# Optimization experiments

Measured on AMD Instinct MI355X. Metric: run time of the kernel, lower is better.

The kernel has to match this reference:

```python
import jax, jax.numpy as jnp
import numpy as np

B, S, D, H = 4, 2048, 2048, 16
HD = D // H  # 128, even -> odd-padding branch in rotate_pos_encode is inactive


def rope(x, base):
    # x: [..., S, Dh], Dh even. freqs_len = (Dh+1)//2 == Dh//2
    Dh = x.shape[-1]
    half = (Dh + 1) // 2
    f = 1.0 / base ** (jnp.arange(half, dtype=jnp.float32) / half)
    ang = jnp.arange(x.shape[-2], dtype=jnp.float32)[:, None] * f[None, :]  # [S, half]
    cos, sin = jnp.cos(ang), jnp.sin(ang)
    xr = x.reshape(*x.shape[:-1], half, 2)
    x0, x1 = xr[..., 0], xr[..., 1]
    # complex multiply (x0 + i x1) * (cos + i sin)
    out = jnp.stack([x0 * cos - x1 * sin, x0 * sin + x1 * cos], axis=-1)
    return out.reshape(x.shape)


def setup_inputs() -> dict:
    key = jax.random.key(0)
    ks = jax.random.split(key, 8)
    sc = 1.0 / np.sqrt(D)
    return {
        "subject_tokens": jax.random.normal(ks[0], (B, S, D), jnp.float32),
        "object_tokens": jax.random.normal(ks[1], (B, S, D), jnp.float32),
        "wq": jax.random.normal(ks[2], (D, D), jnp.float32) * sc,
        "bq": jnp.zeros((D,), jnp.float32),
        "wk": jax.random.normal(ks[3], (D, D), jnp.float32) * sc,
        "bk": jnp.zeros((D,), jnp.float32),
        "wv": jax.random.normal(ks[4], (D, D), jnp.float32) * sc,
        "bv": jnp.zeros((D,), jnp.float32),
        "wc": jax.random.normal(ks[5], (D, D), jnp.float32) * sc,
        "bc": jnp.zeros((D,), jnp.float32),
        "rotate_base": 10000.0,
        "msk": jnp.tril(jnp.ones((S, S), jnp.int32)),  # causal mask
    }


def _split_heads(x):
    # [B, S, D] -> [B, H, S, HD]
    return x.reshape(*x.shape[:-1], H, HD).swapaxes(-3, -2)


def reference(subject_tokens, object_tokens, wq, bq, wk, bk, wv, bv, wc, bc, rotate_base, msk):
    q = _split_heads(subject_tokens @ wq + bq)
    k = _split_heads(object_tokens @ wk + bk)
    v = _split_heads(object_tokens @ wv + bv)
    q = rope(q, rotate_base)
    k = rope(k, rotate_base)
    a = jnp.einsum('bhsd,bhtd->bhst', q, k) / jnp.sqrt(jnp.float32(HD))
    a = jnp.where(msk == 0, jnp.float32(-1e9), a)
    a = jax.nn.softmax(a, axis=-1)  # dropout is identity in eval mode
    c = jnp.einsum('bhst,bhtd->bhsd', a, v)
    c = c.swapaxes(-3, -2).reshape(*subject_tokens.shape[:-1], H * HD)
    return c @ wc + bc
```

## Files before the change

kernel.cpp:

```cpp
#include <hip/hip_runtime.h>
#include <hip/hip_bf16.h>
#include <math.h>

#define BB 4
#define SS 2048
#define DD 2048
#define HH 16
#define HDIM 128
#define MM (BB * SS)

typedef __attribute__((ext_vector_type(8))) __bf16 bf16x8;
typedef __attribute__((ext_vector_type(4))) float f32x4;

__device__ __forceinline__ void gload_lds16(const void* g, void* l) {
  __builtin_amdgcn_global_load_lds(
      (const __attribute__((address_space(1))) void*)g,
      (__attribute__((address_space(3))) void*)l, 16, 0, 0);
}

__device__ __forceinline__ unsigned short f2us(float x) {
  __hip_bfloat16 h = __float2bfloat16(x);
  return *reinterpret_cast<unsigned short*>(&h);
}

__global__ void detect_cfg(const unsigned int* __restrict__ subj,
                           const unsigned short* __restrict__ rb,
                           unsigned int* __restrict__ cfg) {
  if (threadIdx.x != 0) return;
  int hits = 0;
  for (int i = 0; i < 128; ++i) {
    unsigned int e = (subj[i] >> 7) & 0xFF;
    if (e >= 0x68 && e <= 0x88) ++hits;
  }
  int flagF32 = (hits < 64) ? 1 : 0;

  float c32 = __uint_as_float(((const unsigned int*)rb)[0]);
  float c64;
  {
    unsigned long long u = ((const unsigned long long*)rb)[0];
    c64 = (float)__longlong_as_double((long long)u);
  }
  float c16 = __uint_as_float(((unsigned int)rb[0]) << 16);
  auto ok = [](float x) { return x >= 2.0f && x <= 1.0e8f; };
  float base;
  if (flagF32)
    base = ok(c32) ? c32 : (ok(c64) ? c64 : (ok(c16) ? c16 : 10000.0f));
  else
    base = ok(c16) ? c16 : (ok(c32) ? c32 : (ok(c64) ? c64 : 10000.0f));

  cfg[0] = (unsigned int)flagF32;
  ((float*)cfg)[1] = base;
}

__global__ __launch_bounds__(256) void conv_bf16(
    const void* __restrict__ src, unsigned short* __restrict__ dst,
    long long n8, const unsigned int* __restrict__ cfg) {
  long long i = (long long)blockIdx.x * 256 + threadIdx.x;
  if (i >= n8) return;
  if (cfg[0]) {
    const float4* s = (const float4*)src;
    float4 a = s[2 * i], b = s[2 * i + 1];
    uint4 o;
    o.x = ((unsigned)f2us(a.y) << 16) | f2us(a.x);
    o.y = ((unsigned)f2us(a.w) << 16) | f2us(a.z);
    o.z = ((unsigned)f2us(b.y) << 16) | f2us(b.x);
    o.w = ((unsigned)f2us(b.w) << 16) | f2us(b.z);
    ((uint4*)dst)[i] = o;
  } else {
    ((uint4*)dst)[i] = ((const uint4*)src)[i];
  }
}

__global__ __launch_bounds__(256) void rope_table(
    const unsigned int* __restrict__ cfg, float* __restrict__ cosT,
    float* __restrict__ sinT) {
  int id = blockIdx.x * 256 + threadIdx.x;
  float base = ((const float*)cfg)[1];
  if (!(base >= 2.0f && base <= 1.0e8f)) base = 10000.0f;
  int s = id >> 6, p = id & 63;
  float f = 1.0f / powf(base, (float)p * (1.0f / 64.0f));
  if (!isfinite(f)) f = 0.0f;
  float ang = (float)s * f;
  cosT[id] = cosf(ang);
  sinT[id] = sinf(ang);
}

__global__ __launch_bounds__(256) void prep_weightT(
    const void* __restrict__ in, unsigned short* __restrict__ out,
    const unsigned int* __restrict__ cfg) {
  __shared__ unsigned short tile[64][65];
  const int tid = threadIdx.x;
  const int bx = blockIdx.x * 64;
  const int by = blockIdx.y * 64;
  const int isF32 = cfg[0];
#pragma unroll
  for (int i = 0; i < 4; ++i) {
    int r = (tid >> 4) + i * 16;
    int c4 = (tid & 15) * 4;
    if (isF32) {
      float4 v = *(const float4*)((const float*)in + (size_t)(by + r) * DD +
                                  bx + c4);
      tile[c4 + 0][r] = f2us(v.x);
      tile[c4 + 1][r] = f2us(v.y);
      tile[c4 + 2][r] = f2us(v.z);
      tile[c4 + 3][r] = f2us(v.w);
    } else {
      ushort4 v = *(const ushort4*)((const unsigned short*)in +
                                    (size_t)(by + r) * DD + bx + c4);
      tile[c4 + 0][r] = v.x;
      tile[c4 + 1][r] = v.y;
      tile[c4 + 2][r] = v.z;
      tile[c4 + 3][r] = v.w;
    }
  }
  __syncthreads();
#pragma unroll
  for (int i = 0; i < 4; ++i) {
    int c = (tid >> 4) + i * 16;
    int r4 = (tid & 15) * 4;
    ushort4 v;
    v.x = tile[c][r4 + 0];
    v.y = tile[c][r4 + 1];
    v.z = tile[c][r4 + 2];
    v.w = tile[c][r4 + 3];
    *(ushort4*)(out + (size_t)(bx + c) * DD + by + r4) = v;
  }
}

__global__ __launch_bounds__(256) void gemm_nt(
    const __hip_bfloat16* __restrict__ A, const __hip_bfloat16* __restrict__ Bt,
    const __hip_bfloat16* __restrict__ bias, const float* __restrict__ ropeCos,
    const float* __restrict__ ropeSin, void* __restrict__ outv, int mode,
    const unsigned int* __restrict__ cfg) {
  __shared__ __hip_bfloat16 Asm_[128 * 64];
  __shared__ __hip_bfloat16 Bsm_[128 * 64];
  const int tid = threadIdx.x;
  const int wave = tid >> 6, lane = tid & 63;
  const int fl = lane & 15, quad = lane >> 4;
  const int wr = (wave >> 1) * 64, wc = (wave & 1) * 64;
  const int m0 = blockIdx.y * 128, n0 = blockIdx.x * 128;

  const __hip_bfloat16* Ab = A + (size_t)m0 * DD;
  const __hip_bfloat16* Bb = Bt + (size_t)n0 * DD;

  f32x4 acc[4][4] = {};

  for (int k0 = 0; k0 < DD; k0 += 64) {
    __syncthreads();
#pragma unroll
    for (int j = 0; j < 4; ++j) {
      int slot = j * 256 + tid;
      int row = slot >> 3;
      int c8 = ((slot & 7) ^ (row & 7)) << 3;
      int dst = j * 4096 + wave * 1024;
      gload_lds16(Ab + (size_t)row * DD + (k0 + c8), (char*)Asm_ + dst);
      gload_lds16(Bb + (size_t)row * DD + (k0 + c8), (char*)Bsm_ + dst);
    }
    asm volatile("s_waitcnt vmcnt(0)" ::: "memory");
    __syncthreads();

#pragma unroll
    for (int kk = 0; kk < 2; ++kk) {
      bf16x8 af[4], bfv[4];
#pragma unroll
      for (int mb = 0; mb < 4; ++mb) {
        int row = wr + mb * 16 + fl;
        int cc = (kk * 4 + quad) ^ (row & 7);
        af[mb] = *(const bf16x8*)(Asm_ + row * 64 + cc * 8);
      }
#pragma unroll
      for (int nb = 0; nb < 4; ++nb) {
        int row = wc + nb * 16 + fl;
        int cc = (kk * 4 + quad) ^ (row & 7);
        bfv[nb] = *(const bf16x8*)(Bsm_ + row * 64 + cc * 8);
      }
#pragma unroll
      for (int mb = 0; mb < 4; ++mb)
#pragma unroll
        for (int nb = 0; nb < 4; ++nb)
          acc[mb][nb] = __builtin_amdgcn_mfma_f32_16x16x32_bf16(
              af[mb], bfv[nb], acc[mb][nb], 0, 0, 0);
    }
  }

  const int outF32 = cfg[0];
#pragma unroll
  for (int mb = 0; mb < 4; ++mb) {
#pragma unroll
    for (int nb = 0; nb < 4; ++nb) {
      int gn = n0 + wc + nb * 16 + fl;
      int gmBase = m0 + wr + mb * 16 + quad * 4;
      float bv = __bfloat162float(bias[gn]);
      if (mode == 0) {
#pragma unroll
        for (int r = 0; r < 4; ++r) {
          float v = acc[mb][nb][r] + bv;
          size_t idx = (size_t)(gmBase + r) * DD + gn;
          if (outF32)
            ((float*)outv)[idx] = v;
          else
            ((__hip_bfloat16*)outv)[idx] = __float2bfloat16(v);
        }
      } else if (mode == 1) {
        __hip_bfloat16* out = (__hip_bfloat16*)outv;
        int p = (gn & 127) >> 1;
        bool odd = gn & 1;
        int h = gn >> 7;
#pragma unroll
        for (int r = 0; r < 4; ++r) {
          int gm = gmBase + r;
          float v = acc[mb][nb][r] + bv;
          float w = __shfl_xor(v, 1);
          int s = gm & (SS - 1), b = gm >> 11;
          float c = ropeCos[s * 64 + p], si = ropeSin[s * 64 + p];
          float res = odd ? (w * si + v * c) : (v * c - w * si);
          size_t idx = (((size_t)b * HH + h) * SS + s) * HDIM + (gn & 127);
          out[idx] = __float2bfloat16(res);
        }
      } else {
        __hip_bfloat16* out = (__hip_bfloat16*)outv;
        int h = gn >> 7, d = gn & 127;
#pragma unroll
        for (int r = 0; r < 4; ++r) {
          int gm = gmBase + r;
          float v = acc[mb][nb][r] + bv;
          int s = gm & (SS - 1), b = gm >> 11;
          size_t idx = (((size_t)b * HH + h) * HDIM + d) * SS + s;
          out[idx] = __float2bfloat16(v);
        }
      }
    }
  }
}

__global__ __launch_bounds__(512) void attn(
    const __hip_bfloat16* __restrict__ Q, const __hip_bfloat16* __restrict__ K,
    const __hip_bfloat16* __restrict__ Vt, __hip_bfloat16* __restrict__ Ctx) {
  __shared__ __hip_bfloat16 Ksm[2][64 * 128];
  __shared__ __hip_bfloat16 Vsm[2][128 * 64];
  __shared__ __hip_bfloat16 Psm[8 * 16 * 64];

  const int tid = threadIdx.x;
  const int wave = tid >> 6, lane = tid & 63;
  const int fl = lane & 15, quad = lane >> 4;
  const int qt = 15 - blockIdx.x;
  const int bh = blockIdx.y;
  const int nkv = 2 * qt + 2;

  const __hip_bfloat16* Qb = Q + (size_t)bh * SS * HDIM;
  const __hip_bfloat16* Kb = K + (size_t)bh * SS * HDIM;
  const __hip_bfloat16* Vb = Vt + (size_t)bh * HDIM * SS;

  auto stage = [&](int kt, int b) {
#pragma unroll
    for (int j = 0; j < 2; ++j) {
      int blk = j * 8 + wave;
      int slot = blk * 64 + lane;
      {
        int t = slot >> 4, ch = slot & 15;
        int c = ch ^ (t & 15);
        gload_lds16(Kb + (size_t)(kt * 64 + t) * HDIM + c * 8,
                    (char*)(&Ksm[b][0]) + blk * 1024);
      }
      {
        int d = slot >> 3, ch = slot & 7;
        int c = ch ^ (d & 7);
        gload_lds16(Vb + (size_t)d * SS + kt * 64 + c * 8,
                    (char*)(&Vsm[b][0]) + blk * 1024);
      }
    }
  };

  bf16x8 qf[4];
  const int qrow = qt * 128 + wave * 16 + fl;
#pragma unroll
  for (int kb = 0; kb < 4; ++kb)
    qf[kb] = *(const bf16x8*)(Qb + (size_t)qrow * HDIM + kb * 32 + quad * 8);

  f32x4 of[8] = {};
  float m_run[4], l_run[4];
#pragma unroll
  for (int r = 0; r < 4; ++r) {
    m_run[r] = -1e30f;
    l_run[r] = 0.f;
  }
  const float scale = 0.08838834764831845f;

  stage(0, 0);
  asm volatile("s_waitcnt vmcnt(0)" ::: "memory");
  __syncthreads();
  int cur = 0;

  for (int kt = 0; kt < nkv; ++kt) {
    if (kt + 1 < nkv) stage(kt + 1, cur ^ 1);
    const __hip_bfloat16* Ks = &Ksm[cur][0];
    const __hip_bfloat16* Vs = &Vsm[cur][0];

    const int qlo = qt * 128 + wave * 16;
    const bool skipw = (kt * 64) > (qlo + 15);
    const bool maskt = (kt * 64 + 63) > qlo;

    if (!skipw) {
      f32x4 sf[4] = {};
#pragma unroll
      for (int nb = 0; nb < 4; ++nb) {
#pragma unroll
        for (int kb = 0; kb < 4; ++kb) {
          int cc = (kb * 4 + quad) ^ fl;
          bf16x8 kf = *(const bf16x8*)(Ks + (nb * 16 + fl) * 128 + cc * 8);
          sf[nb] = __builtin_amdgcn_mfma_f32_16x16x32_bf16(qf[kb], kf, sf[nb],
                                                           0, 0, 0);
        }
      }
#pragma unroll
      for (int nb = 0; nb < 4; ++nb)
#pragma unroll
        for (int r = 0; r < 4; ++r) {
          float v = sf[nb][r] * scale;
          if (maskt) {
            int tg = kt * 64 + nb * 16 + fl;
            int qg = qlo + quad * 4 + r;
            if (tg > qg) v = -1e30f;
          }
          sf[nb][r] = v;
        }
      float mx[4];
#pragma unroll
      for (int r = 0; r < 4; ++r)
        mx[r] = fmaxf(fmaxf(sf[0][r], sf[1][r]), fmaxf(sf[2][r], sf[3][r]));
#pragma unroll
      for (int off = 1; off <= 8; off <<= 1)
#pragma unroll
        for (int r = 0; r < 4; ++r)
          mx[r] = fmaxf(mx[r], __shfl_xor(mx[r], off));
      bool need = false;
#pragma unroll
      for (int r = 0; r < 4; ++r) need = need || (mx[r] > m_run[r] + 8.0f);
      if (__any(need)) {
#pragma unroll
        for (int r = 0; r < 4; ++r) {
          float mnew = fmaxf(m_run[r], mx[r]);
          float alpha = __expf(m_run[r] - mnew);
          m_run[r] = mnew;
          l_run[r] *= alpha;
#pragma unroll
          for (int nb = 0; nb < 8; ++nb) of[nb][r] *= alpha;
        }
      }
      float rs[4] = {0.f, 0.f, 0.f, 0.f};
#pragma unroll
      for (int nb = 0; nb < 4; ++nb)
#pragma unroll
        for (int r = 0; r < 4; ++r) {
          float p = __expf(sf[nb][r] - m_run[r]);
          rs[r] += p;
          int q = quad * 4 + r;
          int t = nb * 16 + fl;
          int cc = (t >> 3) ^ (q & 7);
          Psm[wave * 1024 + q * 64 + cc * 8 + (t & 7)] = __float2bfloat16(p);
        }
#pragma unroll
      for (int off = 1; off <= 8; off <<= 1)
#pragma unroll
        for (int r = 0; r < 4; ++r) rs[r] += __shfl_xor(rs[r], off);
#pragma unroll
      for (int r = 0; r < 4; ++r) l_run[r] += rs[r];

      asm volatile("s_waitcnt lgkmcnt(0)" ::: "memory");
#pragma unroll
      for (int kb = 0; kb < 2; ++kb) {
        int pc = (kb * 4 + quad) ^ (fl & 7);
        bf16x8 pf = *(const bf16x8*)(Psm + wave * 1024 + fl * 64 + pc * 8);
#pragma unroll
        for (int nb = 0; nb < 8; ++nb) {
          int vc = (kb * 4 + quad) ^ (fl & 7);
          bf16x8 vf = *(const bf16x8*)(Vs + (nb * 16 + fl) * 64 + vc * 8);
          of[nb] =
              __builtin_amdgcn_mfma_f32_16x16x32_bf16(pf, vf, of[nb], 0, 0, 0);
        }
      }
    }

    asm volatile("s_waitcnt vmcnt(0)" ::: "memory");
    __syncthreads();
    cur ^= 1;
  }

  const int b = bh >> 4, h = bh & 15;
#pragma unroll
  for (int nb = 0; nb < 8; ++nb) {
#pragma unroll
    for (int r = 0; r < 4; ++r) {
      int s = qt * 128 + wave * 16 + quad * 4 + r;
      int d = h * HDIM + nb * 16 + fl;
      float v = of[nb][r] / l_run[r];
      Ctx[((size_t)b * SS + s) * DD + d] = __float2bfloat16(v);
    }
  }
}

extern "C" void kernel_launch(void* const* d_in, const int* in_sizes, int n_in,
                              void* d_out, int out_size, void* d_ws,
                              size_t ws_size, hipStream_t stream) {
  const void* subj = d_in[0];
  const void* obj = d_in[1];
  const void* wq = d_in[2];
  const void* bq = d_in[3];
  const void* wk = d_in[4];
  const void* bk = d_in[5];
  const void* wv = d_in[6];
  const void* bv = d_in[7];
  const void* wc = d_in[8];
  const void* bc = d_in[9];
  const unsigned short* rb = (const unsigned short*)d_in[10];

  char* ws = (char*)d_ws;
  const size_t MB = 1024 * 1024;
  unsigned int* cfg = (unsigned int*)ws;
  unsigned short* bqc = (unsigned short*)(ws + 4 * 1024);
  unsigned short* bkc = (unsigned short*)(ws + 8 * 1024);
  unsigned short* bvc = (unsigned short*)(ws + 12 * 1024);
  unsigned short* bcc = (unsigned short*)(ws + 16 * 1024);
  float* ropeCos = (float*)(ws + 1 * MB);
  float* ropeSin = (float*)(ws + 1 * MB + 512 * 1024);
  unsigned short* BufA = (unsigned short*)(ws + 2 * MB);
  unsigned short* BufB = (unsigned short*)(ws + 34 * MB);
  unsigned short* BufC = (unsigned short*)(ws + 66 * MB);
  unsigned short* wT = (unsigned short*)(ws + 98 * MB);

  const long long TOK8 = (long long)MM * DD / 8;

  detect_cfg<<<1, 64, 0, stream>>>((const unsigned int*)subj, rb, cfg);
  rope_table<<<(SS * 64) / 256, 256, 0, stream>>>(cfg, ropeCos, ropeSin);
  conv_bf16<<<8192, 256, 0, stream>>>(subj, BufA, TOK8, cfg);
  conv_bf16<<<8192, 256, 0, stream>>>(obj, BufB, TOK8, cfg);
  conv_bf16<<<1, 256, 0, stream>>>(bq, bqc, 256, cfg);
  conv_bf16<<<1, 256, 0, stream>>>(bk, bkc, 256, cfg);
  conv_bf16<<<1, 256, 0, stream>>>(bv, bvc, 256, cfg);
  conv_bf16<<<1, 256, 0, stream>>>(bc, bcc, 256, cfg);

  prep_weightT<<<dim3(32, 32), 256, 0, stream>>>(wq, wT, cfg);
  gemm_nt<<<dim3(16, 64), 256, 0, stream>>>(
      (const __hip_bfloat16*)BufA, (const __hip_bfloat16*)wT,
      (const __hip_bfloat16*)bqc, ropeCos, ropeSin, d_out, 1, cfg);
  prep_weightT<<<dim3(32, 32), 256, 0, stream>>>(wk, wT, cfg);
  gemm_nt<<<dim3(16, 64), 256, 0, stream>>>(
      (const __hip_bfloat16*)BufB, (const __hip_bfloat16*)wT,
      (const __hip_bfloat16*)bkc, ropeCos, ropeSin, BufA, 1, cfg);
  prep_weightT<<<dim3(32, 32), 256, 0, stream>>>(wv, wT, cfg);
  gemm_nt<<<dim3(16, 64), 256, 0, stream>>>(
      (const __hip_bfloat16*)BufB, (const __hip_bfloat16*)wT,
      (const __hip_bfloat16*)bvc, ropeCos, ropeSin, BufC, 2, cfg);
  attn<<<dim3(16, 64), 512, 0, stream>>>(
      (const __hip_bfloat16*)d_out, (const __hip_bfloat16*)BufA,
      (const __hip_bfloat16*)BufC, (__hip_bfloat16*)BufB);
  prep_weightT<<<dim3(32, 32), 256, 0, stream>>>(wc, wT, cfg);
  gemm_nt<<<dim3(16, 64), 256, 0, stream>>>(
      (const __hip_bfloat16*)BufB, (const __hip_bfloat16*)wT,
      (const __hip_bfloat16*)bcc, ropeCos, ropeSin, d_out, 0, cfg);
}
```

Baseline: 932.4 us.

## Compute transposed scores and pass P via lane shuffles instead of LDS

The attention kernel now computes S^T by swapping the MFMA operands, so each lane holds one query row. Row max and row sum then need only two cross-quad shuffles, and the online-softmax state becomes one scalar per lane. The probabilities are packed to bf16 and rearranged into the PV MFMA A-operand layout with register shuffles, which removes the per-wave LDS P buffer, its stores and the lgkmcnt wait. It also adds a launch-bounds occupancy hint of 4 and replaces the final division with a reciprocal multiply. The cost is many extra ds_bpermute shuffles per tile and more register pressure under the tighter occupancy bound.

Measured after the change: 842.4 us. 1.11x faster.

```diff
diff --git a/kernel.cpp b/kernel.cpp
--- a/kernel.cpp
+++ b/kernel.cpp
@@ -233,12 +233,11 @@
   }
 }
 
-__global__ __launch_bounds__(512) void attn(
+__global__ __launch_bounds__(512, 4) void attn(
     const __hip_bfloat16* __restrict__ Q, const __hip_bfloat16* __restrict__ K,
     const __hip_bfloat16* __restrict__ Vt, __hip_bfloat16* __restrict__ Ctx) {
   __shared__ __hip_bfloat16 Ksm[2][64 * 128];
   __shared__ __hip_bfloat16 Vsm[2][128 * 64];
-  __shared__ __hip_bfloat16 Psm[8 * 16 * 64];
 
   const int tid = threadIdx.x;
   const int wave = tid >> 6, lane = tid & 63;
@@ -278,13 +277,9 @@
     qf[kb] = *(const bf16x8*)(Qb + (size_t)qrow * HDIM + kb * 32 + quad * 8);
 
   f32x4 of[8] = {};
-  float m_run[4], l_run[4];
-#pragma unroll
-  for (int r = 0; r < 4; ++r) {
-    m_run[r] = -1e30f;
-    l_run[r] = 0.f;
-  }
+  float m_run = -1e30f, l_run = 0.f;
   const float scale = 0.08838834764831845f;
+  const int tq0 = quad & 1, tq1 = quad >> 1;
 
   stage(0, 0);
   asm volatile("s_waitcnt vmcnt(0)" ::: "memory");
@@ -301,82 +296,89 @@
     const bool maskt = (kt * 64 + 63) > qlo;
 
     if (!skipw) {
-      f32x4 sf[4] = {};
+      f32x4 st[4] = {};
 #pragma unroll
       for (int nb = 0; nb < 4; ++nb) {
 #pragma unroll
         for (int kb = 0; kb < 4; ++kb) {
           int cc = (kb * 4 + quad) ^ fl;
           bf16x8 kf = *(const bf16x8*)(Ks + (nb * 16 + fl) * 128 + cc * 8);
-          sf[nb] = __builtin_amdgcn_mfma_f32_16x16x32_bf16(qf[kb], kf, sf[nb],
+          st[nb] = __builtin_amdgcn_mfma_f32_16x16x32_bf16(kf, qf[kb], st[nb],
                                                            0, 0, 0);
         }
       }
+      const int qg = qlo + fl;
 #pragma unroll
       for (int nb = 0; nb < 4; ++nb)
 #pragma unroll
         for (int r = 0; r < 4; ++r) {
-          float v = sf[nb][r] * scale;
+          float v = st[nb][r] * scale;
           if (maskt) {
-            int tg = kt * 64 + nb * 16 + fl;
-            int qg = qlo + quad * 4 + r;
+            int tg = kt * 64 + nb * 16 + quad * 4 + r;
             if (tg > qg) v = -1e30f;
           }
-          sf[nb][r] = v;
-        }
-      float mx[4];
-#pragma unroll
-      for (int r = 0; r < 4; ++r)
-        mx[r] = fmaxf(fmaxf(sf[0][r], sf[1][r]), fmaxf(sf[2][r], sf[3][r]));
-#pragma unroll
-      for (int off = 1; off <= 8; off <<= 1)
+          st[nb][r] = v;
+        }
+      float mx = st[0][0];
+#pragma unroll
+      for (int nb = 0; nb < 4; ++nb)
+#pragma unroll
+        for (int r = 0; r < 4; ++r) mx = fmaxf(mx, st[nb][r]);
+      mx = fmaxf(mx, __shfl_xor(mx, 16));
+      mx = fmaxf(mx, __shfl_xor(mx, 32));
+      if (__any(mx > m_run + 8.0f)) {
+        float mnew = fmaxf(m_run, mx);
+        float alpha = __expf(m_run - mnew);
+        m_run = mnew;
+        l_run *= alpha;
+        float al[4];
 #pragma unroll
         for (int r = 0; r < 4; ++r)
-          mx[r] = fmaxf(mx[r], __shfl_xor(mx[r], off));
-      bool need = false;
-#pragma unroll
-      for (int r = 0; r < 4; ++r) need = need || (mx[r] > m_run[r] + 8.0f);
-      if (__any(need)) {
+          al[r] = __shfl(alpha, (quad << 4) + quad * 4 + r);
+#pragma unroll
+        for (int nb = 0; nb < 8; ++nb)
+#pragma unroll
+          for (int r = 0; r < 4; ++r) of[nb][r] *= al[r];
+      }
+      float rsum = 0.f;
+#pragma unroll
+      for (int nb = 0; nb < 4; ++nb)
 #pragma unroll
         for (int r = 0; r < 4; ++r) {
-          float mnew = fmaxf(m_run[r], mx[r]);
-          float alpha = __expf(m_run[r] - mnew);
-          m_run[r] = mnew;
-          l_run[r] *= alpha;
-#pragma unroll
-          for (int nb = 0; nb < 8; ++nb) of[nb][r] *= alpha;
-        }
-      }
-      float rs[4] = {0.f, 0.f, 0.f, 0.f};
-#pragma unroll
-      for (int nb = 0; nb < 4; ++nb)
-#pragma unroll
-        for (int r = 0; r < 4; ++r) {
-          float p = __expf(sf[nb][r] - m_run[r]);
-          rs[r] += p;
-          int q = quad * 4 + r;
-          int t = nb * 16 + fl;
-          int cc = (t >> 3) ^ (q & 7);
-          Psm[wave * 1024 + q * 64 + cc * 8 + (t & 7)] = __float2bfloat16(p);
-        }
-#pragma unroll
-      for (int off = 1; off <= 8; off <<= 1)
-#pragma unroll
-        for (int r = 0; r < 4; ++r) rs[r] += __shfl_xor(rs[r], off);
-#pragma unroll
-      for (int r = 0; r < 4; ++r) l_run[r] += rs[r];
-
-      asm volatile("s_waitcnt lgkmcnt(0)" ::: "memory");
+          float p = __expf(st[nb][r] - m_run);
+          st[nb][r] = p;
+          rsum += p;
+        }
+      rsum += __shfl_xor(rsum, 16);
+      rsum += __shfl_xor(rsum, 32);
+      l_run += rsum;
+      unsigned int pk[4][2];
+#pragma unroll
+      for (int nb = 0; nb < 4; ++nb) {
+        pk[nb][0] = ((unsigned)f2us(st[nb][1]) << 16) | f2us(st[nb][0]);
+        pk[nb][1] = ((unsigned)f2us(st[nb][3]) << 16) | f2us(st[nb][2]);
+      }
+      union PAU {
+        unsigned int u[4];
+        bf16x8 v;
+      } pa[2];
+#pragma unroll
+      for (int kb = 0; kb < 2; ++kb)
+#pragma unroll
+        for (int w = 0; w < 4; ++w) {
+          int src = fl + 16 * ((tq0 << 1) | (w >> 1));
+          unsigned int v0 = (unsigned int)__shfl((int)pk[kb * 2 + 0][w & 1], src);
+          unsigned int v1 = (unsigned int)__shfl((int)pk[kb * 2 + 1][w & 1], src);
+          pa[kb].u[w] = tq1 ? v1 : v0;
+        }
 #pragma unroll
       for (int kb = 0; kb < 2; ++kb) {
-        int pc = (kb * 4 + quad) ^ (fl & 7);
-        bf16x8 pf = *(const bf16x8*)(Psm + wave * 1024 + fl * 64 + pc * 8);
 #pragma unroll
         for (int nb = 0; nb < 8; ++nb) {
           int vc = (kb * 4 + quad) ^ (fl & 7);
           bf16x8 vf = *(const bf16x8*)(Vs + (nb * 16 + fl) * 64 + vc * 8);
-          of[nb] =
-              __builtin_amdgcn_mfma_f32_16x16x32_bf16(pf, vf, of[nb], 0, 0, 0);
+          of[nb] = __builtin_amdgcn_mfma_f32_16x16x32_bf16(pa[kb].v, vf,
+                                                           of[nb], 0, 0, 0);
         }
       }
     }
@@ -386,6 +388,12 @@
     cur ^= 1;
   }
 
+  float lr[4];
+#pragma unroll
+  for (int r = 0; r < 4; ++r) {
+    float l = __shfl(l_run, (quad << 4) + quad * 4 + r);
+    lr[r] = 1.0f / l;
+  }
   const int b = bh >> 4, h = bh & 15;
 #pragma unroll
   for (int nb = 0; nb < 8; ++nb) {
@@ -393,7 +401,7 @@
     for (int r = 0; r < 4; ++r) {
       int s = qt * 128 + wave * 16 + quad * 4 + r;
       int d = h * HDIM + nb * 16 + fl;
-      float v = of[nb][r] / l_run[r];
+      float v = of[nb][r] * lr[r];
       Ctx[((size_t)b * SS + s) * DD + d] = __float2bfloat16(v);
     }
   }
```
